# Kernel tuning notes

Measured on AMD Instinct MI355X. Metric: run time of the kernel, lower is better.

Reference implementation:

```python
import jax, jax.numpy as jnp
import numpy as np
import math

D = 128       # d_model (file-scope constant)
L_LEN = 128   # length; forced == d_model by the un-transposed attention call
NH = 4        # n_head
DK = D // NH
K = 7         # depthwise conv kernel size
LC = 4        # conv_num
EPS = 1e-5    # LayerNorm eps
NEG = -1e30


def _pos_encoding():
    i = np.arange(D).astype(np.float64)
    freqs = np.where(i % 2 == 0, 10000.0 ** (-i / D), -(10000.0 ** ((1 - i) / D)))
    phases = np.where(i % 2 == 0, 0.0, math.pi / 2)
    pos = np.arange(L_LEN).astype(np.float64)[None, :]          # (1, L)
    pe = np.sin(pos * freqs[:, None] + phases[:, None])          # (D, L)
    return jnp.asarray(pe, jnp.float32)

PE = _pos_encoding()


def layernorm2d(x, w, b):
    # LayerNorm over the trailing (D, L) dims jointly, elementwise affine (D, L)
    mu = x.mean(axis=(-2, -1), keepdims=True)
    var = x.var(axis=(-2, -1), keepdims=True)
    return (x - mu) * jax.lax.rsqrt(var + EPS) * w + b


def sep_conv(x, dw_w, dw_b, pw_w, pw_b):
    # depthwise conv1d (groups=C) then 1x1 pointwise conv. x: (B, C, L)
    h = jax.lax.conv_general_dilated(
        x, dw_w[:, None, :], window_strides=(1,), padding=[(K // 2, K // 2)],
        dimension_numbers=('NCH', 'OIH', 'NCH'), feature_group_count=D)
    h = h + dw_b[:, None]
    return jnp.einsum('bcl,oc->bol', h, pw_w) + pw_b[:, None]


def mha(x, mask_f, Wq, bq, Wk, bk, Wv, bv, Wo, bo):
    # x: (B, Lx, F) with Lx == F == D here (module feeds (B, d_model, length) untransposed)
    B, Lx, _ = x.shape
    q = (x @ Wq.T + bq).reshape(B, Lx, NH, DK)
    k = (x @ Wk.T + bk).reshape(B, Lx, NH, DK)
    v = (x @ Wv.T + bv).reshape(B, Lx, NH, DK)
    scores = jnp.einsum('bqhd,bkhd->bhqk', q, k) * (1.0 / math.sqrt(DK))
    m = mask_f[:, None, None, :]                         # (B,1,1,Lx)
    scores = scores * (1.0 - m) + m * NEG                # mask_logits
    attn = jax.nn.softmax(scores, axis=-1)
    out = jnp.einsum('bhqk,bkhd->bqhd', attn, v).reshape(B, Lx, D)
    return out @ Wo.T + bo


def setup_inputs() -> dict:
    key = jax.random.key(0)
    ks = jax.random.split(key, 16)
    B = 1024
    s = 0.02
    inp = {
        'x': jax.random.normal(ks[0], (B, D, L_LEN), jnp.float32),
        'mask': jax.random.randint(ks[1], (B, L_LEN), 0, 2, jnp.int32),
        'dw_w': jax.random.normal(ks[2], (LC, D, K), jnp.float32) * s,
        'dw_b': jnp.zeros((LC, D), jnp.float32),
        'pw_w': jax.random.normal(ks[3], (LC, D, D), jnp.float32) * s,
        'pw_b': jnp.zeros((LC, D), jnp.float32),
        'normb_w': jnp.ones((D, L_LEN), jnp.float32),
        'normb_b': jnp.zeros((D, L_LEN), jnp.float32),
        'norms_w': jnp.ones((LC, D, L_LEN), jnp.float32),
        'norms_b': jnp.zeros((LC, D, L_LEN), jnp.float32),
        'norme_w': jnp.ones((D, L_LEN), jnp.float32),
        'norme_b': jnp.zeros((D, L_LEN), jnp.float32),
        'Wq': jax.random.normal(ks[4], (D, D), jnp.float32) * s,
        'bq': jnp.zeros((D,), jnp.float32),
        'Wk': jax.random.normal(ks[5], (D, D), jnp.float32) * s,
        'bk': jnp.zeros((D,), jnp.float32),
        'Wv': jax.random.normal(ks[6], (D, D), jnp.float32) * s,
        'bv': jnp.zeros((D,), jnp.float32),
        'Wo': jax.random.normal(ks[7], (D, D), jnp.float32) * s,
        'bo': jnp.zeros((D,), jnp.float32),
        'fc_w': jax.random.normal(ks[8], (D, D), jnp.float32) * s,
        'fc_b': jnp.zeros((D,), jnp.float32),
    }
    return inp


def reference(x, mask, dw_w, dw_b, pw_w, pw_b, normb_w, normb_b, norms_w, norms_b,
              norme_w, norme_b, Wq, bq, Wk, bk, Wv, bv, Wo, bo, fc_w, fc_b):
    # Eval mode: all dropouts are identity.
    mask_f = mask.astype(x.dtype)
    out = x + PE                                  # PosEncoder
    res = out
    out = layernorm2d(out, normb_w, normb_b)      # normb
    for i in range(LC):                           # fixed small layer loop
        h = sep_conv(out, dw_w[i], dw_b[i], pw_w[i], pw_b[i])
        out = jax.nn.relu(h) + res
        res = out
        out = layernorm2d(out, norms_w[i], norms_b[i])
    att = mha(out, mask_f, Wq, bq, Wk, bk, Wv, bv, Wo, bo)
    out = att + res
    res = out
    out = layernorm2d(out, norme_w, norme_b)
    # fc applied over channel dim: (B,C,L)->(B,L,C) linear ->(B,C,L)
    h = jnp.einsum('bcl,oc->bol', out, fc_w) + fc_b[:, None]
    out = jax.nn.relu(h) + res
    return out
```

## Files before the change

kernel.cpp:

```cpp
#include <hip/hip_runtime.h>

#define NEGF -1e30f
#define EPSF 1e-5f

typedef __attribute__((ext_vector_type(8))) short bf16x8;
typedef __attribute__((ext_vector_type(4))) float f32x4;
typedef unsigned short u16;
typedef unsigned int u32;

#define WSU_PW 0
#define WSU_FC 65536
#define WSU_WO 81920
#define WSU_WQ 98304
#define WSU_WK 114688
#define WSU_WV 131072
#define WSU_END 147456

__device__ __forceinline__ u16 f2bf(float x) {
  u32 u = __float_as_uint(x);
  u += 0x7fffu + ((u >> 16) & 1u);
  return (u16)(u >> 16);
}
__device__ __forceinline__ float bf2f(u16 u) {
  return __uint_as_float(((u32)u) << 16);
}
__device__ __forceinline__ f32x4 mfma16(bf16x8 a, bf16x8 b, f32x4 c) {
  return __builtin_amdgcn_mfma_f32_16x16x32_bf16(a, b, c, 0, 0, 0);
}
__device__ __forceinline__ void mm_frags(const u16* base, bf16x8* f) {
  f[0] = *(const bf16x8*)(base);
  f[1] = *(const bf16x8*)(base + 32);
  f[2] = *(const bf16x8*)(base + 64);
  f[3] = *(const bf16x8*)(base + 96);
}

__global__ __launch_bounds__(128) void prep_kernel(
    const float* __restrict__ pw_w, const float* __restrict__ fc_w,
    const float* __restrict__ Wo, const float* __restrict__ Wq,
    const float* __restrict__ Wk, const float* __restrict__ Wv,
    u16* __restrict__ wsu) {
  int job = blockIdx.x, r = blockIdx.y, c = threadIdx.x;
  int idx = r * 128 + c;
  if (job < 4)       wsu[WSU_PW + job * 16384 + idx] = f2bf(pw_w[job * 16384 + idx]);
  else if (job == 4) wsu[WSU_FC + idx] = f2bf(fc_w[idx]);
  else if (job == 5) wsu[WSU_WO + idx] = f2bf(Wo[idx]);
  else if (job == 6) wsu[WSU_WQ + idx] = f2bf(Wq[idx]);
  else if (job == 7) wsu[WSU_WK + idx] = f2bf(Wk[idx]);
  else if (job == 8) wsu[WSU_WV + idx] = f2bf(Wv[idx]);
  else {
    float* pe = (float*)(wsu + WSU_END);
    int d = r, pos = c;
    double freq, phase;
    if ((d & 1) == 0) { freq = pow(10000.0, -(double)d / 128.0); phase = 0.0; }
    else { freq = -pow(10000.0, (1.0 - (double)d) / 128.0); phase = 1.5707963267948966; }
    pe[d * 128 + pos] = (float)sin((double)pos * freq + phase);
  }
}

__device__ __forceinline__ void ln_stats(const float* resv, float* red, int t,
                                         float& mu, float& inv) {
  float s = 0.f, s2 = 0.f;
#pragma unroll
  for (int i = 0; i < 16; i++) { float v = resv[i]; s += v; s2 += v * v; }
#pragma unroll
  for (int off = 32; off > 0; off >>= 1) {
    s += __shfl_down(s, off, 64);
    s2 += __shfl_down(s2, off, 64);
  }
  if ((t & 63) == 0) { red[(t >> 6) * 2] = s; red[(t >> 6) * 2 + 1] = s2; }
  __syncthreads();
  float S = 0.f, S2 = 0.f;
#pragma unroll
  for (int i = 0; i < 16; i++) { S += red[2 * i]; S2 += red[2 * i + 1]; }
  mu = S * (1.0f / 16384.0f);
  float var = S2 * (1.0f / 16384.0f) - mu * mu;
  inv = rsqrtf(var + EPSF);
}

__global__ __launch_bounds__(1024) void enc_kernel(
    const float* __restrict__ x, const int* __restrict__ mask,
    const float* __restrict__ dw_w, const float* __restrict__ dw_b,
    const float* __restrict__ pw_b,
    const float* __restrict__ normb_w, const float* __restrict__ normb_b,
    const float* __restrict__ norms_w, const float* __restrict__ norms_b,
    const float* __restrict__ norme_w, const float* __restrict__ norme_b,
    const float* __restrict__ bq, const float* __restrict__ bk,
    const float* __restrict__ bv, const float* __restrict__ bo,
    const float* __restrict__ fc_b, const u16* __restrict__ wsu,
    const float* __restrict__ pe, float* __restrict__ out) {
  __shared__ __align__(16) u16 A_raw[128 * 136 + 16];
  __shared__ __align__(16) u16 B_[27136];
  __shared__ float mask_s[128];
  __shared__ float red[32];
  u16* A = A_raw + 8;
  u16* QH = B_;
  u16* KH = B_ + 9216;
  u16* VT = B_ + 18432;
  u16* PN = B_;

  const int t = threadIdx.x;
  const int b = blockIdx.x;
  const int lane = t & 63;
  const int r16 = lane & 15;
  const int quad = lane >> 4;
  const int wv = t >> 6;
  const int m0 = __builtin_amdgcn_readfirstlane((wv >> 1) << 4);
  const int nh = __builtin_amdgcn_readfirstlane(wv & 1);
  const int l = t & 127;
  const int og = __builtin_amdgcn_readfirstlane(t >> 7);
  const int obase = og << 4;
  const int hh = __builtin_amdgcn_readfirstlane(wv >> 3);
  const int mq0 = __builtin_amdgcn_readfirstlane((wv & 7) << 4);

  if (t < 128) mask_s[t] = (float)mask[b * 128 + t];

  float res[16];
  {
    const float* xb = x + (size_t)b * 16384;
#pragma unroll
    for (int i = 0; i < 16; i++) {
      int o = obase + i;
      res[i] = xb[o * 128 + l] + pe[o * 128 + l];
    }
  }
  {
    float mu, inv;
    ln_stats(res, red, t, mu, inv);
#pragma unroll
    for (int i = 0; i < 16; i++) {
      int o = obase + i;
      A[o * 136 + l] = f2bf((res[i] - mu) * inv * normb_w[o * 128 + l] + normb_b[o * 128 + l]);
    }
    __syncthreads();
  }

#pragma unroll 1
  for (int layer = 0; layer < 4; layer++) {
    {
      const float* dwp = dw_w + layer * 896 + l * 7;
      float wreg[7];
#pragma unroll
      for (int j = 0; j < 7; j++) wreg[j] = dwp[j];
      float bias = dw_b[layer * 128 + l];
      const u16* xrow = A + l * 136;
#pragma unroll
      for (int k = 0; k < 2; k++) {
        const int lb = (og << 4) + 8 * k;
        bf16x8 vz = {0, 0, 0, 0, 0, 0, 0, 0};
        bf16x8 vc = *(const bf16x8*)(xrow + lb);
        bf16x8 vp = (lb == 0) ? vz : *(const bf16x8*)(xrow + lb - 8);
        bf16x8 vn = (lb == 120) ? vz : *(const bf16x8*)(xrow + lb + 8);
        float w14[14];
        w14[0] = bf2f((u16)vp[5]); w14[1] = bf2f((u16)vp[6]); w14[2] = bf2f((u16)vp[7]);
#pragma unroll
        for (int j = 0; j < 8; j++) w14[3 + j] = bf2f((u16)vc[j]);
        w14[11] = bf2f((u16)vn[0]); w14[12] = bf2f((u16)vn[1]); w14[13] = bf2f((u16)vn[2]);
#pragma unroll
        for (int j = 0; j < 8; j++) {
          float a = bias;
#pragma unroll
          for (int tt = 0; tt < 7; tt++) a += w14[j + tt] * wreg[tt];
          B_[(lb + j) * 136 + l] = f2bf(a);
        }
      }
    }
    __syncthreads();
    {
      const u16* pwp = wsu + WSU_PW + (layer << 14) + (m0 + r16) * 128 + quad * 8;
      bf16x8 a[4];
      mm_frags(pwp, a);
#pragma unroll
      for (int ni = 0; ni < 4; ni++) {
        int n = nh * 4 + ni;
        const u16* hb = B_ + (16 * n + r16) * 136 + quad * 8;
        f32x4 c = {0.f, 0.f, 0.f, 0.f};
        c = mfma16(a[0], *(const bf16x8*)(hb), c);
        c = mfma16(a[1], *(const bf16x8*)(hb + 32), c);
        c = mfma16(a[2], *(const bf16x8*)(hb + 64), c);
        c = mfma16(a[3], *(const bf16x8*)(hb + 96), c);
        u16* sp = A + (m0 + quad * 4) * 136 + 16 * n + r16;
        sp[0] = f2bf(c[0]); sp[136] = f2bf(c[1]); sp[272] = f2bf(c[2]); sp[408] = f2bf(c[3]);
      }
    }
    __syncthreads();
    {
#pragma unroll
      for (int i = 0; i < 16; i++)
        res[i] += fmaxf(bf2f(A[(obase + i) * 136 + l]) + pw_b[layer * 128 + obase + i], 0.f);
      float mu, inv;
      ln_stats(res, red, t, mu, inv);
      const float* wg = norms_w + layer * 16384;
      const float* bg = norms_b + layer * 16384;
#pragma unroll
      for (int i = 0; i < 16; i++) {
        int o = obase + i;
        A[o * 136 + l] = f2bf((res[i] - mu) * inv * wg[o * 128 + l] + bg[o * 128 + l]);
      }
      __syncthreads();
    }
  }

  float att[16];
#pragma unroll
  for (int p = 0; p < 2; p++) {
    {
      const u16* xp = A + (m0 + r16) * 136 + quad * 8;
      bf16x8 xf[4];
      mm_frags(xp, xf);
#pragma unroll
      for (int ni = 0; ni < 2; ni++) {
        const int nt = nh * 2 + ni;
        const int j2 = nt * 16 + r16;
        const int jrow = p * 64 + j2;
        {
          bf16x8 w[4];
          mm_frags(wsu + WSU_WQ + jrow * 128 + quad * 8, w);
          f32x4 c = {0.f, 0.f, 0.f, 0.f};
          c = mfma16(xf[0], w[0], c); c = mfma16(xf[1], w[1], c);
          c = mfma16(xf[2], w[2], c); c = mfma16(xf[3], w[3], c);
          float bb = bq[jrow];
#pragma unroll
          for (int r = 0; r < 4; r++)
            QH[(m0 + quad * 4 + r) * 72 + j2] = f2bf((c[r] + bb) * 0.17677669529663687f);
        }
        {
          bf16x8 w[4];
          mm_frags(wsu + WSU_WK + jrow * 128 + quad * 8, w);
          f32x4 c = {0.f, 0.f, 0.f, 0.f};
          c = mfma16(xf[0], w[0], c); c = mfma16(xf[1], w[1], c);
          c = mfma16(xf[2], w[2], c); c = mfma16(xf[3], w[3], c);
          float bb = bk[jrow];
#pragma unroll
          for (int r = 0; r < 4; r++)
            KH[(m0 + quad * 4 + r) * 72 + j2] = f2bf(c[r] + bb);
        }
        {
          bf16x8 w[4];
          mm_frags(wsu + WSU_WV + jrow * 128 + quad * 8, w);
          f32x4 c = {0.f, 0.f, 0.f, 0.f};
          c = mfma16(xf[0], w[0], c); c = mfma16(xf[1], w[1], c);
          c = mfma16(xf[2], w[2], c); c = mfma16(xf[3], w[3], c);
          float bb = bv[jrow];
          u32 lo = (u32)f2bf(c[0] + bb) | ((u32)f2bf(c[1] + bb) << 16);
          u32 hi = (u32)f2bf(c[2] + bb) | ((u32)f2bf(c[3] + bb) << 16);
          u16* vp = VT + j2 * 136 + m0 + quad * 4;
          *(u32*)(vp) = lo;
          *(u32*)(vp + 2) = hi;
        }
      }
    }
    __syncthreads();
    f32x4 sc[8];
    {
      bf16x8 aq = *(const bf16x8*)(QH + (mq0 + r16) * 72 + hh * 32 + quad * 8);
#pragma unroll
      for (int n = 0; n < 8; n++) {
        f32x4 z = {0.f, 0.f, 0.f, 0.f};
        sc[n] = mfma16(aq, *(const bf16x8*)(KH + (16 * n + r16) * 72 + hh * 32 + quad * 8), z);
      }
    }
    __syncthreads();
    float linv[4];
    {
      float mv[8];
#pragma unroll
      for (int n = 0; n < 8; n++) mv[n] = mask_s[16 * n + r16];
#pragma unroll
      for (int r = 0; r < 4; r++) {
        float sv[8];
#pragma unroll
        for (int n = 0; n < 8; n++) sv[n] = (mv[n] > 0.5f) ? NEGF : sc[n][r];
        float mx = sv[0];
#pragma unroll
        for (int n = 1; n < 8; n++) mx = fmaxf(mx, sv[n]);
        mx = fmaxf(mx, __shfl_xor(mx, 1, 64));
        mx = fmaxf(mx, __shfl_xor(mx, 2, 64));
        mx = fmaxf(mx, __shfl_xor(mx, 4, 64));
        mx = fmaxf(mx, __shfl_xor(mx, 8, 64));
        float sum = 0.f;
#pragma unroll
        for (int n = 0; n < 8; n++) { float pp = __expf(sv[n] - mx); sv[n] = pp; sum += pp; }
        sum += __shfl_xor(sum, 1, 64);
        sum += __shfl_xor(sum, 2, 64);
        sum += __shfl_xor(sum, 4, 64);
        sum += __shfl_xor(sum, 8, 64);
        linv[r] = 1.0f / sum;
        u16* pp = PN + (mq0 + quad * 4 + r) * 136 + r16;
#pragma unroll
        for (int n = 0; n < 8; n++) pp[16 * n] = f2bf(sv[n]);
      }
    }
    {
      const u16* pq = PN + (mq0 + r16) * 136 + quad * 8;
      bf16x8 pf[4];
      mm_frags(pq, pf);
#pragma unroll
      for (int nv = 0; nv < 2; nv++) {
        const u16* vb = VT + (hh * 32 + nv * 16 + r16) * 136 + quad * 8;
        f32x4 c = {0.f, 0.f, 0.f, 0.f};
        c = mfma16(pf[0], *(const bf16x8*)(vb), c);
        c = mfma16(pf[1], *(const bf16x8*)(vb + 32), c);
        c = mfma16(pf[2], *(const bf16x8*)(vb + 64), c);
        c = mfma16(pf[3], *(const bf16x8*)(vb + 96), c);
#pragma unroll
        for (int r = 0; r < 4; r++) att[p * 8 + nv * 4 + r] = c[r] * linv[r];
      }
    }
    __syncthreads();
  }

#pragma unroll
  for (int p = 0; p < 2; p++)
#pragma unroll
    for (int nv = 0; nv < 2; nv++)
#pragma unroll
      for (int r = 0; r < 4; r++)
        A[(mq0 + quad * 4 + r) * 136 + (2 * p + hh) * 32 + nv * 16 + r16] =
            f2bf(att[p * 8 + nv * 4 + r]);
  __syncthreads();
  {
    const u16* ap = A + (m0 + r16) * 136 + quad * 8;
    bf16x8 a[4];
    mm_frags(ap, a);
#pragma unroll
    for (int ni = 0; ni < 4; ni++) {
      int n = nh * 4 + ni;
      bf16x8 w[4];
      mm_frags(wsu + WSU_WO + (16 * n + r16) * 128 + quad * 8, w);
      f32x4 c = {0.f, 0.f, 0.f, 0.f};
      c = mfma16(a[0], w[0], c); c = mfma16(a[1], w[1], c);
      c = mfma16(a[2], w[2], c); c = mfma16(a[3], w[3], c);
      u16* sp = B_ + (m0 + quad * 4) * 136 + 16 * n + r16;
      sp[0] = f2bf(c[0]); sp[136] = f2bf(c[1]); sp[272] = f2bf(c[2]); sp[408] = f2bf(c[3]);
    }
  }
  __syncthreads();
  {
    float bol = bo[l];
#pragma unroll
    for (int i = 0; i < 16; i++) res[i] += bf2f(B_[(obase + i) * 136 + l]) + bol;
    float mu, inv;
    ln_stats(res, red, t, mu, inv);
#pragma unroll
    for (int i = 0; i < 16; i += 2) {
      int o = obase + i;
      float v0 = (res[i] - mu) * inv * norme_w[o * 128 + l] + norme_b[o * 128 + l];
      float v1 = (res[i + 1] - mu) * inv * norme_w[(o + 1) * 128 + l] + norme_b[(o + 1) * 128 + l];
      *(u32*)(A + l * 136 + o) = (u32)f2bf(v0) | ((u32)f2bf(v1) << 16);
    }
    __syncthreads();
  }
  {
    const u16* fp = wsu + WSU_FC + (m0 + r16) * 128 + quad * 8;
    bf16x8 a[4];
    mm_frags(fp, a);
#pragma unroll
    for (int ni = 0; ni < 4; ni++) {
      int n = nh * 4 + ni;
      const u16* hb = A + (16 * n + r16) * 136 + quad * 8;
      f32x4 c = {0.f, 0.f, 0.f, 0.f};
      c = mfma16(a[0], *(const bf16x8*)(hb), c);
      c = mfma16(a[1], *(const bf16x8*)(hb + 32), c);
      c = mfma16(a[2], *(const bf16x8*)(hb + 64), c);
      c = mfma16(a[3], *(const bf16x8*)(hb + 96), c);
      u16* sp = B_ + (m0 + quad * 4) * 136 + 16 * n + r16;
      sp[0] = f2bf(c[0]); sp[136] = f2bf(c[1]); sp[272] = f2bf(c[2]); sp[408] = f2bf(c[3]);
    }
  }
  __syncthreads();
  {
    float* outb = out + (size_t)b * 16384;
#pragma unroll
    for (int i = 0; i < 16; i++) {
      float hv = bf2f(B_[(obase + i) * 136 + l]) + fc_b[obase + i];
      outb[(obase + i) * 128 + l] = fmaxf(hv, 0.f) + res[i];
    }
  }
}

extern "C" void kernel_launch(void* const* d_in, const int* in_sizes, int n_in,
                              void* d_out, int out_size, void* d_ws, size_t ws_size,
                              hipStream_t stream) {
  const float* x       = (const float*)d_in[0];
  const int*   mask    = (const int*)d_in[1];
  const float* dw_w    = (const float*)d_in[2];
  const float* dw_b    = (const float*)d_in[3];
  const float* pw_w    = (const float*)d_in[4];
  const float* pw_b    = (const float*)d_in[5];
  const float* normb_w = (const float*)d_in[6];
  const float* normb_b = (const float*)d_in[7];
  const float* norms_w = (const float*)d_in[8];
  const float* norms_b = (const float*)d_in[9];
  const float* norme_w = (const float*)d_in[10];
  const float* norme_b = (const float*)d_in[11];
  const float* Wq      = (const float*)d_in[12];
  const float* bq      = (const float*)d_in[13];
  const float* Wk      = (const float*)d_in[14];
  const float* bk      = (const float*)d_in[15];
  const float* Wv      = (const float*)d_in[16];
  const float* bv      = (const float*)d_in[17];
  const float* Wo      = (const float*)d_in[18];
  const float* bo      = (const float*)d_in[19];
  const float* fc_w    = (const float*)d_in[20];
  const float* fc_b    = (const float*)d_in[21];
  float* out = (float*)d_out;
  u16* wsu = (u16*)d_ws;
  const float* pe = (const float*)(wsu + WSU_END);
  int B = in_sizes[0] / 16384;

  prep_kernel<<<dim3(10, 128), dim3(128), 0, stream>>>(pw_w, fc_w, Wo, Wq, Wk, Wv, wsu);
  enc_kernel<<<dim3(B), dim3(1024), 0, stream>>>(
      x, mask, dw_w, dw_b, pw_b, normb_w, normb_b, norms_w, norms_b,
      norme_w, norme_b, bq, bk, bv, bo, fc_b, wsu, pe, out);
}
```

Measured before the change: 584.0 us.

## Process attention one head per pass with duplicated softmax across wave halves

Restructures the attention stage from two passes of two heads each into four passes of one head. The two wave groups now both compute the same head's scores and softmax, each writing half of the probability row, then each computes half of the head's output dims. This shrinks the Q/K/V shared-memory buffers, which could allow more resident blocks per CU. In exchange it doubles the number of pass iterations and barriers, adds an extra __syncthreads, and duplicates the QK^T and softmax work.

```diff
diff --git a/kernel.cpp b/kernel.cpp
--- a/kernel.cpp
+++ b/kernel.cpp
@@ -89,13 +89,13 @@
     const float* __restrict__ fc_b, const u16* __restrict__ wsu,
     const float* __restrict__ pe, float* __restrict__ out) {
   __shared__ __align__(16) u16 A_raw[128 * 136 + 16];
-  __shared__ __align__(16) u16 B_[27136];
+  __shared__ __align__(16) u16 B_[21760];
   __shared__ float mask_s[128];
   __shared__ float red[32];
   u16* A = A_raw + 8;
   u16* QH = B_;
-  u16* KH = B_ + 9216;
-  u16* VT = B_ + 18432;
+  u16* KH = B_ + 5120;
+  u16* VT = B_ + 17408;
   u16* PN = B_;
 
   const int t = threadIdx.x;
@@ -109,7 +109,7 @@
   const int l = t & 127;
   const int og = __builtin_amdgcn_readfirstlane(t >> 7);
   const int obase = og << 4;
-  const int hh = __builtin_amdgcn_readfirstlane(wv >> 3);
+  const int dup = __builtin_amdgcn_readfirstlane(wv >> 3);
   const int mq0 = __builtin_amdgcn_readfirstlane((wv & 7) << 4);
 
   if (t < 128) mask_s[t] = (float)mask[b * 128 + t];
@@ -202,61 +202,57 @@
 
   float att[16];
 #pragma unroll
-  for (int p = 0; p < 2; p++) {
+  for (int hd = 0; hd < 4; hd++) {
     {
       const u16* xp = A + (m0 + r16) * 136 + quad * 8;
       bf16x8 xf[4];
       mm_frags(xp, xf);
-#pragma unroll
-      for (int ni = 0; ni < 2; ni++) {
-        const int nt = nh * 2 + ni;
-        const int j2 = nt * 16 + r16;
-        const int jrow = p * 64 + j2;
-        {
-          bf16x8 w[4];
-          mm_frags(wsu + WSU_WQ + jrow * 128 + quad * 8, w);
-          f32x4 c = {0.f, 0.f, 0.f, 0.f};
-          c = mfma16(xf[0], w[0], c); c = mfma16(xf[1], w[1], c);
-          c = mfma16(xf[2], w[2], c); c = mfma16(xf[3], w[3], c);
-          float bb = bq[jrow];
-#pragma unroll
-          for (int r = 0; r < 4; r++)
-            QH[(m0 + quad * 4 + r) * 72 + j2] = f2bf((c[r] + bb) * 0.17677669529663687f);
-        }
-        {
-          bf16x8 w[4];
-          mm_frags(wsu + WSU_WK + jrow * 128 + quad * 8, w);
-          f32x4 c = {0.f, 0.f, 0.f, 0.f};
-          c = mfma16(xf[0], w[0], c); c = mfma16(xf[1], w[1], c);
-          c = mfma16(xf[2], w[2], c); c = mfma16(xf[3], w[3], c);
-          float bb = bk[jrow];
-#pragma unroll
-          for (int r = 0; r < 4; r++)
-            KH[(m0 + quad * 4 + r) * 72 + j2] = f2bf(c[r] + bb);
-        }
-        {
-          bf16x8 w[4];
-          mm_frags(wsu + WSU_WV + jrow * 128 + quad * 8, w);
-          f32x4 c = {0.f, 0.f, 0.f, 0.f};
-          c = mfma16(xf[0], w[0], c); c = mfma16(xf[1], w[1], c);
-          c = mfma16(xf[2], w[2], c); c = mfma16(xf[3], w[3], c);
-          float bb = bv[jrow];
-          u32 lo = (u32)f2bf(c[0] + bb) | ((u32)f2bf(c[1] + bb) << 16);
-          u32 hi = (u32)f2bf(c[2] + bb) | ((u32)f2bf(c[3] + bb) << 16);
-          u16* vp = VT + j2 * 136 + m0 + quad * 4;
-          *(u32*)(vp) = lo;
-          *(u32*)(vp + 2) = hi;
-        }
+      const int j2 = nh * 16 + r16;
+      const int jrow = hd * 32 + j2;
+      {
+        bf16x8 w[4];
+        mm_frags(wsu + WSU_WQ + jrow * 128 + quad * 8, w);
+        f32x4 c = {0.f, 0.f, 0.f, 0.f};
+        c = mfma16(xf[0], w[0], c); c = mfma16(xf[1], w[1], c);
+        c = mfma16(xf[2], w[2], c); c = mfma16(xf[3], w[3], c);
+        float bb = bq[jrow];
+#pragma unroll
+        for (int r = 0; r < 4; r++)
+          QH[(m0 + quad * 4 + r) * 40 + j2] = f2bf((c[r] + bb) * 0.17677669529663687f);
+      }
+      {
+        bf16x8 w[4];
+        mm_frags(wsu + WSU_WK + jrow * 128 + quad * 8, w);
+        f32x4 c = {0.f, 0.f, 0.f, 0.f};
+        c = mfma16(xf[0], w[0], c); c = mfma16(xf[1], w[1], c);
+        c = mfma16(xf[2], w[2], c); c = mfma16(xf[3], w[3], c);
+        float bb = bk[jrow];
+#pragma unroll
+        for (int r = 0; r < 4; r++)
+          KH[(m0 + quad * 4 + r) * 40 + j2] = f2bf(c[r] + bb);
+      }
+      {
+        bf16x8 w[4];
+        mm_frags(wsu + WSU_WV + jrow * 128 + quad * 8, w);
+        f32x4 c = {0.f, 0.f, 0.f, 0.f};
+        c = mfma16(xf[0], w[0], c); c = mfma16(xf[1], w[1], c);
+        c = mfma16(xf[2], w[2], c); c = mfma16(xf[3], w[3], c);
+        float bb = bv[jrow];
+        u32 lo = (u32)f2bf(c[0] + bb) | ((u32)f2bf(c[1] + bb) << 16);
+        u32 hi = (u32)f2bf(c[2] + bb) | ((u32)f2bf(c[3] + bb) << 16);
+        u16* vp = VT + j2 * 136 + m0 + quad * 4;
+        *(u32*)(vp) = lo;
+        *(u32*)(vp + 2) = hi;
       }
     }
     __syncthreads();
     f32x4 sc[8];
     {
-      bf16x8 aq = *(const bf16x8*)(QH + (mq0 + r16) * 72 + hh * 32 + quad * 8);
+      bf16x8 aq = *(const bf16x8*)(QH + (mq0 + r16) * 40 + quad * 8);
 #pragma unroll
       for (int n = 0; n < 8; n++) {
         f32x4 z = {0.f, 0.f, 0.f, 0.f};
-        sc[n] = mfma16(aq, *(const bf16x8*)(KH + (16 * n + r16) * 72 + hh * 32 + quad * 8), z);
+        sc[n] = mfma16(aq, *(const bf16x8*)(KH + (16 * n + r16) * 40 + quad * 8), z);
       }
     }
     __syncthreads();
@@ -285,38 +281,38 @@
         sum += __shfl_xor(sum, 4, 64);
         sum += __shfl_xor(sum, 8, 64);
         linv[r] = 1.0f / sum;
-        u16* pp = PN + (mq0 + quad * 4 + r) * 136 + r16;
-#pragma unroll
-        for (int n = 0; n < 8; n++) pp[16 * n] = f2bf(sv[n]);
-      }
-    }
+        u16* pp2 = PN + (mq0 + quad * 4 + r) * 136 + r16;
+        if (dup == 0) {
+          pp2[0] = f2bf(sv[0]); pp2[16] = f2bf(sv[1]);
+          pp2[32] = f2bf(sv[2]); pp2[48] = f2bf(sv[3]);
+        } else {
+          pp2[64] = f2bf(sv[4]); pp2[80] = f2bf(sv[5]);
+          pp2[96] = f2bf(sv[6]); pp2[112] = f2bf(sv[7]);
+        }
+      }
+    }
+    __syncthreads();
     {
       const u16* pq = PN + (mq0 + r16) * 136 + quad * 8;
       bf16x8 pf[4];
       mm_frags(pq, pf);
-#pragma unroll
-      for (int nv = 0; nv < 2; nv++) {
-        const u16* vb = VT + (hh * 32 + nv * 16 + r16) * 136 + quad * 8;
-        f32x4 c = {0.f, 0.f, 0.f, 0.f};
-        c = mfma16(pf[0], *(const bf16x8*)(vb), c);
-        c = mfma16(pf[1], *(const bf16x8*)(vb + 32), c);
-        c = mfma16(pf[2], *(const bf16x8*)(vb + 64), c);
-        c = mfma16(pf[3], *(const bf16x8*)(vb + 96), c);
-#pragma unroll
-        for (int r = 0; r < 4; r++) att[p * 8 + nv * 4 + r] = c[r] * linv[r];
-      }
-    }
-    __syncthreads();
-  }
-
-#pragma unroll
-  for (int p = 0; p < 2; p++)
-#pragma unroll
-    for (int nv = 0; nv < 2; nv++)
-#pragma unroll
-      for (int r = 0; r < 4; r++)
-        A[(mq0 + quad * 4 + r) * 136 + (2 * p + hh) * 32 + nv * 16 + r16] =
-            f2bf(att[p * 8 + nv * 4 + r]);
+      const u16* vb = VT + (dup * 16 + r16) * 136 + quad * 8;
+      f32x4 c = {0.f, 0.f, 0.f, 0.f};
+      c = mfma16(pf[0], *(const bf16x8*)(vb), c);
+      c = mfma16(pf[1], *(const bf16x8*)(vb + 32), c);
+      c = mfma16(pf[2], *(const bf16x8*)(vb + 64), c);
+      c = mfma16(pf[3], *(const bf16x8*)(vb + 96), c);
+#pragma unroll
+      for (int r = 0; r < 4; r++) att[hd * 4 + r] = c[r] * linv[r];
+    }
+    __syncthreads();
+  }
+
+#pragma unroll
+  for (int hd = 0; hd < 4; hd++)
+#pragma unroll
+    for (int r = 0; r < 4; r++)
+      A[(mq0 + quad * 4 + r) * 136 + hd * 32 + dup * 16 + r16] = f2bf(att[hd * 4 + r]);
   __syncthreads();
   {
     const u16* ap = A + (m0 + r16) * 136 + quad * 8;
```

Measured after the change: 615.0 us. 5.3% more time.
